# Kernel optimization log

Hardware: AMD Instinct MI355X
Metric: run time of the kernel (lower is better)

Reference implementation:

```python
import jax, jax.numpy as jnp
import numpy as np
import math

L_MAX = 16  # matches init_kwargs; output has (L_MAX+1)**2 columns, sphericart ordering l*l+l+m
N_POINTS = 500000


def _prefactors(l_max):
    # F_l^m = (-1)^m * sqrt((2l+1)/(2*pi) * (l-m)!/(l+m)!)  (sphericart convention)
    F = {}
    for l in range(l_max + 1):
        for m in range(l + 1):
            F[(l, m)] = ((-1.0) ** m) * math.sqrt(
                (2 * l + 1) / (2.0 * math.pi) * math.factorial(l - m) / math.factorial(l + m)
            )
    return F


def _solid_harmonics(xyz, l_max):
    # Scaled (solid) real spherical harmonics \tilde{Y}_l^m = r^l Y_l^m, sphericart normalized=False.
    x, y, z = xyz[:, 0], xyz[:, 1], xyz[:, 2]
    r2 = x * x + y * y + z * z
    dt = xyz.dtype
    one = jnp.ones_like(x)

    # c_m + i s_m = (x + i y)^m
    c = [one]
    s = [jnp.zeros_like(x)]
    for m in range(1, l_max + 1):
        c.append(x * c[m - 1] - y * s[m - 1])
        s.append(x * s[m - 1] + y * c[m - 1])

    # Modified associated Legendre recurrence (in z and r^2, polynomial in x,y,z):
    #   Q_0^0 = 1
    #   Q_l^l = -(2l-1) Q_{l-1}^{l-1}
    #   Q_l^{l-1} = (2l-1) z Q_{l-1}^{l-1}
    #   Q_l^m = ((2l-1) z Q_{l-1}^m - (l+m-1) r^2 Q_{l-2}^m) / (l - m)
    Q = {(0, 0): one}
    for l in range(1, l_max + 1):
        Q[(l, l)] = jnp.asarray(-(2 * l - 1), dt) * Q[(l - 1, l - 1)]
        Q[(l, l - 1)] = jnp.asarray(2 * l - 1, dt) * z * Q[(l - 1, l - 1)]
        for m in range(l - 2, -1, -1):
            Q[(l, m)] = (
                jnp.asarray(2 * l - 1, dt) * z * Q[(l - 1, m)]
                - jnp.asarray(l + m - 1, dt) * r2 * Q[(l - 2, m)]
            ) * jnp.asarray(1.0 / (l - m), dt)

    F = _prefactors(l_max)
    inv_sqrt2 = 1.0 / math.sqrt(2.0)
    cols = []
    for l in range(l_max + 1):
        for m in range(-l, l + 1):
            am = abs(m)
            base = jnp.asarray(F[(l, am)], dt) * Q[(l, am)]
            if m < 0:
                cols.append(base * s[am])
            elif m == 0:
                cols.append(base * jnp.asarray(inv_sqrt2, dt))
            else:
                cols.append(base * c[m])
    return jnp.stack(cols, axis=-1)  # [N, (l_max+1)^2]


def setup_inputs() -> dict:
    key = jax.random.key(0)
    xyz = 6.0 * jax.random.normal(key, (N_POINTS, 3), dtype=jnp.float32)
    return {"xyz": xyz}


def reference(xyz):
    return _solid_harmonics(xyz, L_MAX)
```

## Files before the change

kernel.cpp:

```cpp
#include <hip/hip_runtime.h>

#define L_MAX 16
#define NCOL  289
#define BPTS  64

constexpr double csqrt(double x) {
  double g = x > 1.0 ? x : 1.0;
  for (int i = 0; i < 500; ++i) {
    double n = 0.5 * (g + x / g);
    if (n == g) break;
    g = n;
  }
  return g;
}
constexpr double cfact(int n) { double f = 1.0; for (int i = 2; i <= n; ++i) f *= (double)i; return f; }

struct FTab { float v[L_MAX + 1][L_MAX + 1]; };
constexpr FTab make_ftab() {
  FTab t{};
  for (int l = 0; l <= L_MAX; ++l)
    for (int m = 0; m <= l; ++m) {
      double val = ((m & 1) ? -1.0 : 1.0) *
        csqrt((2.0 * l + 1.0) / (2.0 * 3.14159265358979323846) * cfact(l - m) / cfact(l + m));
      t.v[l][m] = (float)val;
    }
  return t;
}
constexpr FTab FT = make_ftab();

__global__ __launch_bounds__(64)
void sh_kernel(const float* __restrict__ xyz, float* __restrict__ out, int npts) {
  __shared__ float lds[BPTS * NCOL];

  const int  lane   = threadIdx.x;
  const int  batch  = blockIdx.x;
  const long long p0 = (long long)batch * BPTS;
  const int  nvalid = min(BPTS, npts - (int)p0);
  const int  p      = (int)p0 + lane;

  if (lane < nvalid) {
    const float x = xyz[3 * p + 0];
    const float y = xyz[3 * p + 1];
    const float z = xyz[3 * p + 2];
    const float r2 = x * x + y * y + z * z;
    float* row = &lds[lane * NCOL];

    float cc[L_MAX + 1], ss[L_MAX + 1];
    cc[0] = 1.f; ss[0] = 0.f;
#pragma unroll
    for (int m = 1; m <= L_MAX; ++m) {
      cc[m] = x * cc[m - 1] - y * ss[m - 1];
      ss[m] = x * ss[m - 1] + y * cc[m - 1];
    }

    constexpr float INVS2 = 0.70710678118654752440f;

    float Qm1[L_MAX + 1], Qm2[L_MAX + 1], cur[L_MAX + 1];
    Qm1[0] = 1.f;
    row[0] = FT.v[0][0] * INVS2;
#pragma unroll
    for (int l = 1; l <= L_MAX; ++l) {
      const float tl = (float)(2 * l - 1);
      cur[l]     = -tl * Qm1[l - 1];
      cur[l - 1] = tl * z * Qm1[l - 1];
#pragma unroll
      for (int m = l - 2; m >= 0; --m)
        cur[m] = (tl * z * Qm1[m] - (float)(l + m - 1) * r2 * Qm2[m]) * (1.f / (float)(l - m));

      const int base = l * l + l;
      row[base] = FT.v[l][0] * cur[0] * INVS2;
#pragma unroll
      for (int m = 1; m <= l; ++m) {
        const float b = FT.v[l][m] * cur[m];
        row[base - m] = b * ss[m];
        row[base + m] = b * cc[m];
      }
#pragma unroll
      for (int m = 0; m <= l; ++m) { Qm2[m] = Qm1[m]; Qm1[m] = cur[m]; }
    }
  }
  __syncthreads();

  const int ndw = nvalid * NCOL;
  float* dst = out + p0 * NCOL;
  const int nv4 = ndw & ~3;
  for (int base = lane * 4; base < nv4; base += 4 * BPTS) {
    float4 v = *reinterpret_cast<const float4*>(&lds[base]);
    *reinterpret_cast<float4*>(&dst[base]) = v;
  }
  for (int i = nv4 + lane; i < ndw; i += BPTS) dst[i] = lds[i];
}

extern "C" void kernel_launch(void* const* d_in, const int* in_sizes, int n_in,
                              void* d_out, int out_size, void* d_ws, size_t ws_size,
                              hipStream_t stream) {
  const float* xyz = (const float*)d_in[0];
  float* out = (float*)d_out;
  const int npts = in_sizes[0] / 3;
  const int nblocks = (npts + BPTS - 1) / BPTS;
  sh_kernel<<<nblocks, BPTS, 0, stream>>>(xyz, out, npts);
}
```

Before: 601.8 us.

## Stage output in column chunks through small LDS buffer with larger blocks

Rather than holding all 289 columns for 64 points in LDS, the kernel now computes the harmonics in l-chunks, each at most 49 columns wide, for 256 points per block. Each chunk goes to a padded LDS tile (odd stride to avoid bank conflicts) and is written out with coalesced scalar stores before the next chunk starts. This cuts the LDS footprint so more waves fit per CU and latency hiding improves. In exchange it adds eight block-wide barriers per block, integer division in the copy loop, and drops the float4 stores.

```diff
diff --git a/kernel.cpp b/kernel.cpp
--- a/kernel.cpp
+++ b/kernel.cpp
@@ -2,7 +2,7 @@
 
 #define L_MAX 16
 #define NCOL  289
-#define BPTS  64
+#define TPB   256
 
 constexpr double csqrt(double x) {
   double g = x > 1.0 ? x : 1.0;
@@ -27,68 +27,97 @@
   return t;
 }
 constexpr FTab FT = make_ftab();
+constexpr float INVS2 = 0.70710678118654752440f;
 
-__global__ __launch_bounds__(64)
-void sh_kernel(const float* __restrict__ xyz, float* __restrict__ out, int npts) {
-  __shared__ float lds[BPTS * NCOL];
+using Arr = float[L_MAX + 1];
 
-  const int  lane   = threadIdx.x;
-  const int  batch  = blockIdx.x;
-  const long long p0 = (long long)batch * BPTS;
-  const int  nvalid = min(BPTS, npts - (int)p0);
-  const int  p      = (int)p0 + lane;
+template<int L>
+__device__ __forceinline__ void qrow(float z, float r2, Arr& Qp, Arr& Qpp, Arr& cur) {
+  constexpr float tl = (float)(2 * L - 1);
+  cur[L]     = -tl * Qp[L - 1];
+  cur[L - 1] =  tl * z * Qp[L - 1];
+#pragma unroll
+  for (int m = L - 2; m >= 0; --m)
+    cur[m] = (tl * z * Qp[m] - (float)(L + m - 1) * r2 * Qpp[m]) * (1.f / (float)(L - m));
+#pragma unroll
+  for (int m = 0; m < L; ++m) Qpp[m] = Qp[m];
+#pragma unroll
+  for (int m = 0; m <= L; ++m) Qp[m] = cur[m];
+}
 
-  if (lane < nvalid) {
-    const float x = xyz[3 * p + 0];
-    const float y = xyz[3 * p + 1];
-    const float z = xyz[3 * p + 2];
-    const float r2 = x * x + y * y + z * z;
-    float* row = &lds[lane * NCOL];
+template<int L, int C0, int WP>
+__device__ __forceinline__ void emit(float* __restrict__ row, const Arr& cc, const Arr& ss, const Arr& cur) {
+  constexpr int base = L * L + L - C0;
+  row[base] = FT.v[L][0] * cur[0] * INVS2;
+#pragma unroll
+  for (int m = 1; m <= L; ++m) {
+    const float b = FT.v[L][m] * cur[m];
+    row[base - m] = b * ss[m];
+    row[base + m] = b * cc[m];
+  }
+}
 
-    float cc[L_MAX + 1], ss[L_MAX + 1];
-    cc[0] = 1.f; ss[0] = 0.f;
-#pragma unroll
-    for (int m = 1; m <= L_MAX; ++m) {
-      cc[m] = x * cc[m - 1] - y * ss[m - 1];
-      ss[m] = x * ss[m - 1] + y * cc[m - 1];
-    }
+template<int L, int L1, int C0, int WP>
+__device__ __forceinline__ void lrun(float z, float r2, float* __restrict__ row,
+                                     const Arr& cc, const Arr& ss, Arr& Qp, Arr& Qpp, Arr& cur) {
+  if constexpr (L == 0) { cur[0] = 1.f; Qp[0] = 1.f; }
+  else qrow<L>(z, r2, Qp, Qpp, cur);
+  emit<L, C0, WP>(row, cc, ss, cur);
+  if constexpr (L < L1) lrun<L + 1, L1, C0, WP>(z, r2, row, cc, ss, Qp, Qpp, cur);
+}
 
-    constexpr float INVS2 = 0.70710678118654752440f;
-
-    float Qm1[L_MAX + 1], Qm2[L_MAX + 1], cur[L_MAX + 1];
-    Qm1[0] = 1.f;
-    row[0] = FT.v[0][0] * INVS2;
-#pragma unroll
-    for (int l = 1; l <= L_MAX; ++l) {
-      const float tl = (float)(2 * l - 1);
-      cur[l]     = -tl * Qm1[l - 1];
-      cur[l - 1] = tl * z * Qm1[l - 1];
-#pragma unroll
-      for (int m = l - 2; m >= 0; --m)
-        cur[m] = (tl * z * Qm1[m] - (float)(l + m - 1) * r2 * Qm2[m]) * (1.f / (float)(l - m));
-
-      const int base = l * l + l;
-      row[base] = FT.v[l][0] * cur[0] * INVS2;
-#pragma unroll
-      for (int m = 1; m <= l; ++m) {
-        const float b = FT.v[l][m] * cur[m];
-        row[base - m] = b * ss[m];
-        row[base + m] = b * cc[m];
-      }
-#pragma unroll
-      for (int m = 0; m <= l; ++m) { Qm2[m] = Qm1[m]; Qm1[m] = cur[m]; }
-    }
+template<int L0, int L1>
+__device__ __forceinline__ void do_chunk(float* __restrict__ lds, int tid, int nvalid,
+                                         float* __restrict__ dst, float z, float r2,
+                                         const Arr& cc, const Arr& ss, Arr& Qp, Arr& Qpp, Arr& cur) {
+  constexpr int C0 = L0 * L0;
+  constexpr int W  = (L1 + 1) * (L1 + 1) - C0;
+  constexpr int WP = W | 1;
+  lrun<L0, L1, C0, WP>(z, r2, lds + tid * WP, cc, ss, Qp, Qpp, cur);
+  __syncthreads();
+  const int ndw = nvalid * W;
+  for (int i = tid; i < ndw; i += TPB) {
+    const int r = i / W;
+    const int c = i - r * W;
+    dst[r * NCOL + C0 + c] = lds[r * WP + c];
   }
   __syncthreads();
+}
 
-  const int ndw = nvalid * NCOL;
-  float* dst = out + p0 * NCOL;
-  const int nv4 = ndw & ~3;
-  for (int base = lane * 4; base < nv4; base += 4 * BPTS) {
-    float4 v = *reinterpret_cast<const float4*>(&lds[base]);
-    *reinterpret_cast<float4*>(&dst[base]) = v;
+__global__ __launch_bounds__(TPB, 3)
+void sh_kernel(const float* __restrict__ xyz, float* __restrict__ out, int npts) {
+  __shared__ float lds[TPB * 49];
+  const int tid = threadIdx.x;
+  const long long p0 = (long long)blockIdx.x * TPB;
+  const int nvalid = min(TPB, (int)(npts - p0));
+
+  float x = 0.f, y = 0.f, z = 0.f;
+  if (tid < nvalid) {
+    const long long p = p0 + tid;
+    x = xyz[3 * p + 0];
+    y = xyz[3 * p + 1];
+    z = xyz[3 * p + 2];
   }
-  for (int i = nv4 + lane; i < ndw; i += BPTS) dst[i] = lds[i];
+  const float r2 = x * x + y * y + z * z;
+
+  Arr cc, ss, Qp, Qpp, cur;
+  cc[0] = 1.f; ss[0] = 0.f;
+#pragma unroll
+  for (int m = 1; m <= L_MAX; ++m) {
+    cc[m] = x * cc[m - 1] - y * ss[m - 1];
+    ss[m] = x * ss[m - 1] + y * cc[m - 1];
+  }
+
+  float* dst = out + (size_t)p0 * NCOL;
+
+  do_chunk< 0,  5>(lds, tid, nvalid, dst, z, r2, cc, ss, Qp, Qpp, cur);
+  do_chunk< 6,  8>(lds, tid, nvalid, dst, z, r2, cc, ss, Qp, Qpp, cur);
+  do_chunk< 9, 10>(lds, tid, nvalid, dst, z, r2, cc, ss, Qp, Qpp, cur);
+  do_chunk<11, 12>(lds, tid, nvalid, dst, z, r2, cc, ss, Qp, Qpp, cur);
+  do_chunk<13, 13>(lds, tid, nvalid, dst, z, r2, cc, ss, Qp, Qpp, cur);
+  do_chunk<14, 14>(lds, tid, nvalid, dst, z, r2, cc, ss, Qp, Qpp, cur);
+  do_chunk<15, 15>(lds, tid, nvalid, dst, z, r2, cc, ss, Qp, Qpp, cur);
+  do_chunk<16, 16>(lds, tid, nvalid, dst, z, r2, cc, ss, Qp, Qpp, cur);
 }
 
 extern "C" void kernel_launch(void* const* d_in, const int* in_sizes, int n_in,
@@ -97,6 +126,6 @@
   const float* xyz = (const float*)d_in[0];
   float* out = (float*)d_out;
   const int npts = in_sizes[0] / 3;
-  const int nblocks = (npts + BPTS - 1) / BPTS;
-  sh_kernel<<<nblocks, BPTS, 0, stream>>>(xyz, out, npts);
+  const int nblocks = (npts + TPB - 1) / TPB;
+  sh_kernel<<<nblocks, TPB, 0, stream>>>(xyz, out, npts);
 }
```

Measured after the change: 765.6 us. +27.2%, slower.
